# Performance work log

Hardware: AMD Instinct MI355X
Metric: run time of the kernel (lower is better)

The kernel has to match this reference:

```python
import jax, jax.numpy as jnp
import numpy as np

N = 50000      # nodes
E = 800000     # edges
IN = 64        # in_channels
HID = 256      # hidden_dim
LAT = 64       # latent_dim
KS = 2         # kernel_size per dim
DIM = 3        # pseudo-coordinate dim
K = KS ** DIM  # 8 spline weight matrices


def spline_basis_coeffs(pseudo, ks, dim, dtype):
    """Degree-1 open B-spline basis: returns per-edge coefficients c [E, ks**dim]."""
    e = pseudo.shape[0]
    v = pseudo * (ks - 1)                                   # [E, dim]
    bot = jnp.clip(jnp.floor(v), 0, ks - 1).astype(jnp.int32)
    frac = v - bot
    c = jnp.zeros((e, ks ** dim), dtype)
    rows = jnp.arange(e)
    for s in range(2 ** dim):  # 8 knot combinations (fixed small loop)
        w = jnp.ones(e, dtype)
        idx = jnp.zeros(e, jnp.int32)
        for d in range(dim):
            bit = (s >> d) & 1
            w = w * (frac[:, d] if bit else 1.0 - frac[:, d])
            idx = idx + jnp.clip(bot[:, d] + bit, 0, ks - 1) * (ks ** d)
        c = c.at[rows, idx].add(w)
    return c


def spline_conv(x, edge_index, pseudo, W, Wroot, b):
    """SplineConv with aggr='mean', root weight and bias (degree-1 open splines)."""
    src, dst = edge_index[0], edge_index[1]
    n = x.shape[0]
    e = pseudo.shape[0]
    c = spline_basis_coeffs(pseudo, KS, DIM, x.dtype)        # [E, K]
    x_src = x[src]                                           # [E, in] gather
    deg = jax.ops.segment_sum(jnp.ones(e, x.dtype), dst, num_segments=n)
    inv_deg = (1.0 / jnp.maximum(deg, 1.0))[:, None]         # [N, 1] mean aggr
    out = jnp.zeros((n, W.shape[2]), x.dtype)
    for k in range(W.shape[0]):  # K=8 fixed loop; scatter-add then dense matmul
        agg = jax.ops.segment_sum(c[:, k:k + 1] * x_src, dst, num_segments=n)
        out = out + (agg * inv_deg) @ W[k]
    return out + x @ Wroot + b


def setup_inputs() -> dict:
    key = jax.random.key(0)
    ks = jax.random.split(key, 12)
    x = jax.random.normal(ks[0], (N, IN), jnp.float32)
    edge_index = jax.random.randint(ks[1], (2, E), 0, N, jnp.int32)
    s = 0.05
    return {
        "x": x,
        "edge_index": edge_index,
        "conv1_W": jax.random.normal(ks[2], (K, IN, HID), jnp.float32) * s,
        "conv1_root": jax.random.normal(ks[3], (IN, HID), jnp.float32) * s,
        "conv1_b": jnp.zeros((HID,), jnp.float32),
        "conv2_W": jax.random.normal(ks[4], (K, HID, LAT), jnp.float32) * s,
        "conv2_root": jax.random.normal(ks[5], (HID, LAT), jnp.float32) * s,
        "conv2_b": jnp.zeros((LAT,), jnp.float32),
        "dec_w1": jax.random.normal(ks[6], (LAT, HID), jnp.float32) * s,
        "dec_b1": jnp.zeros((HID,), jnp.float32),
        "dec_w2": jax.random.normal(ks[7], (HID, IN), jnp.float32) * s,
        "dec_b2": jnp.zeros((IN,), jnp.float32),
    }


def reference(x, edge_index, conv1_W, conv1_root, conv1_b,
              conv2_W, conv2_root, conv2_b,
              dec_w1, dec_b1, dec_w2, dec_b2):
    pseudo = jnp.zeros((edge_index.shape[1], DIM), x.dtype)  # forward builds zeros
    h = jax.nn.relu(spline_conv(x, edge_index, pseudo, conv1_W, conv1_root, conv1_b))
    z = spline_conv(h, edge_index, pseudo, conv2_W, conv2_root, conv2_b)
    h2 = jax.nn.relu(z @ dec_w1 + dec_b1)
    return h2 @ dec_w2 + dec_b2
```

## Files before the change

### kernel.cpp

```cpp
#include <hip/hip_runtime.h>
#include <hip/hip_bf16.h>


#define THREADS 256

typedef __attribute__((ext_vector_type(8))) short bf16x8;
typedef __attribute__((ext_vector_type(4))) float f32x4;

__device__ __forceinline__ float bf2f(unsigned short u) {
    unsigned v = ((unsigned)u) << 16;
    return __builtin_bit_cast(float, v);
}
__device__ __forceinline__ unsigned short f2bf(float f) {
    __hip_bfloat16 h = __float2bfloat16(f);
    return __builtin_bit_cast(unsigned short, h);
}
__device__ __forceinline__ void acc4(float* f, uint2 v) {
    f[0] += bf2f((unsigned short)v.x);
    f[1] += bf2f((unsigned short)(v.x >> 16));
    f[2] += bf2f((unsigned short)v.y);
    f[3] += bf2f((unsigned short)(v.y >> 16));
}

__device__ __forceinline__ void pack_one(unsigned short* dst,
                                         const float* W0, const float* W1,
                                         int NB, int ksplit, int colsplit,
                                         int ld0, int ld1, int t) {
    int i = t & 7, lane = (t >> 3) & 63, rest = t >> 9;
    int j = rest % NB, s = rest / NB;
    int k = s * 32 + ((lane >> 4) << 3) + i;
    int c = (j << 4) + (lane & 15);
    float v;
    if (c >= colsplit)    v = W1[(size_t)k * ld1 + (c - colsplit)];
    else if (k >= ksplit) v = W1[(size_t)(k - ksplit) * ld1 + c];
    else                  v = W0[(size_t)k * ld0 + c];
    dst[t] = f2bf(v);
}

#define BIG (1 << 30)

__global__ void prep_kernel(const float* __restrict__ W1g, const float* __restrict__ root1,
                            const float* __restrict__ W2g, const float* __restrict__ root2,
                            const float* __restrict__ dw1, const float* __restrict__ dw2,
                            const float* __restrict__ x, const int* __restrict__ dstv,
                            int* __restrict__ bcnt,
                            unsigned short* __restrict__ Pb1,
                            unsigned short* __restrict__ Pb2,
                            unsigned short* __restrict__ Pd1,
                            unsigned short* __restrict__ Pd2,
                            unsigned short* __restrict__ ab1,
                            int n, int E, int pb_pack) {
    if ((int)blockIdx.x >= pb_pack) {
        __shared__ int hist[256];
        int t = threadIdx.x;
        hist[t] = 0;
        __syncthreads();
        int e0 = ((int)blockIdx.x - pb_pack) * 4096;
#pragma unroll
        for (int i = 0; i < 16; ++i) {
            int e = e0 + t + i * 256;
            if (e < E) atomicAdd(&hist[dstv[e] >> 8], 1);
        }
        __syncthreads();
        int h = hist[t];
        if (h) atomicAdd(&bcnt[t], h);
        return;
    }
    int t = blockIdx.x * blockDim.x + threadIdx.x;
    if (t < 32768) {
        pack_one(Pb1, W1g, root1, 16, 64, BIG, 256, 256, t);
    } else if (t < 65536) {
        pack_one(Pb2, W2g, root2, 8, BIG, 64, 64, 64, t - 32768);
    } else if (t < 81920) {
        pack_one(Pd1, dw1, dw1, 16, BIG, BIG, 256, 256, t - 65536);
    } else if (t < 98304) {
        pack_one(Pd2, dw2, dw2, 4, BIG, BIG, 64, 64, t - 81920);
    } else if (t < 98304 + n * 16) {
        int u = t - 98304;
        int row = u >> 4, c4 = (u & 15) * 4;
        float4 v = *(const float4*)(x + (size_t)row * 64 + c4);
        unsigned lo = (unsigned)f2bf(v.x) | ((unsigned)f2bf(v.y) << 16);
        unsigned hi = (unsigned)f2bf(v.z) | ((unsigned)f2bf(v.w) << 16);
        uint2 o; o.x = lo; o.y = hi;
        *(uint2*)(ab1 + (size_t)row * 128 + 64 + c4) = o;
    }
}

__global__ __launch_bounds__(256) void partition_edges(
    const int* __restrict__ src, const int* __restrict__ dst,
    const int* __restrict__ bcnt, int* __restrict__ bcur,
    int* __restrict__ epack, int E) {
    __shared__ int hist[256];
    __shared__ int base[256];
    __shared__ int lcur[256];
    __shared__ int bb[256];
    int t = threadIdx.x;
    hist[t] = 0;
    __syncthreads();
    int e0 = blockIdx.x * 4096;
    int myd[16], mys[16];
#pragma unroll
    for (int i = 0; i < 16; ++i) {
        int e = e0 + t + i * 256;
        int d = (e < E) ? dst[e] : -1;
        mys[i] = (e < E) ? src[e] : 0;
        myd[i] = d;
        if (d >= 0) atomicAdd(&hist[d >> 8], 1);
    }
    int cb = bcnt[t];
    bb[t] = cb;
    __syncthreads();
    for (int off = 1; off < 256; off <<= 1) {
        int xv = (t >= off) ? bb[t - off] : 0;
        __syncthreads();
        bb[t] += xv;
        __syncthreads();
    }
    int bbase_t = bb[t] - cb;
    int h = hist[t];
    if (h > 0) base[t] = bbase_t + atomicAdd(&bcur[t], h);
    lcur[t] = 0;
    __syncthreads();
#pragma unroll
    for (int i = 0; i < 16; ++i) {
        int d = myd[i];
        if (d >= 0) {
            int b = d >> 8;
            int p = atomicAdd(&lcur[b], 1);
            epack[base[b] + p] = ((d & 255) << 20) | mys[i];
        }
    }
}

__global__ __launch_bounds__(256) void bucket_fill2(
    const int* __restrict__ epack, const int* __restrict__ bcnt,
    int* __restrict__ offs, float* __restrict__ invd,
    int* __restrict__ esrc, int N) {
    __shared__ int sb_[256];
    __shared__ int nh[256];
    __shared__ int loff[256];
    __shared__ int ncur[256];
    __shared__ int stage[8192];
    int b = blockIdx.x, t = threadIdx.x;
    int n0 = b << 8;
    int cntn = min(256, N - n0);
    int cb = bcnt[t];
    sb_[t] = cb;
    __syncthreads();
    for (int off = 1; off < 256; off <<= 1) {
        int xv = (t >= off) ? sb_[t - off] : 0;
        __syncthreads();
        sb_[t] += xv;
        __syncthreads();
    }
    int ebase = b ? sb_[b - 1] : 0;
    int ecount = sb_[b] - ebase;
    if (b == 0 && t == 0) offs[N] = sb_[255];
    nh[t] = 0;
    __syncthreads();
    for (int i = t; i < ecount; i += 256)
        atomicAdd(&nh[epack[ebase + i] >> 20], 1);
    __syncthreads();
    int v = nh[t];
    loff[t] = v;
    __syncthreads();
    for (int off = 1; off < 256; off <<= 1) {
        int xv = (t >= off) ? loff[t - off] : 0;
        __syncthreads();
        loff[t] += xv;
        __syncthreads();
    }
    int ex = loff[t] - v;
    loff[t] = ex;
    if (t < cntn) {
        offs[n0 + t] = ebase + ex;
        invd[n0 + t] = 1.0f / (float)max(v, 1);
    }
    ncur[t] = 0;
    __syncthreads();
    bool useLds = (ecount <= 8192);
    for (int i = t; i < ecount; i += 256) {
        int p = epack[ebase + i];
        int dl = p >> 20;
        int pos = atomicAdd(&ncur[dl], 1);
        int g = loff[dl] + pos;
        int sv = p & 0xFFFFF;
        if (useLds) stage[g] = sv;
        else        esrc[ebase + g] = sv;
    }
    __syncthreads();
    if (useLds)
        for (int i = t; i < ecount; i += 256) esrc[ebase + i] = stage[i];
}

__global__ void agg_x4(unsigned short* __restrict__ ab1, const int* __restrict__ esrc,
                       const int* __restrict__ offs, const float* __restrict__ invd,
                       int n) {
    int node = blockIdx.x * 4 + (threadIdx.x >> 6);
    if (node >= n) return;
    int l = threadIdx.x & 63;
    int slot = l >> 4, c = l & 15;
    const unsigned short* xb = ab1 + 64 + c * 4;
    int s = offs[node], e = offs[node + 1];
    float a0[4] = {}, a1[4] = {}, a2[4] = {}, a3[4] = {};
    int j = s;
    for (; j + 16 <= e; j += 16) {
        int i0 = esrc[j + slot],      i1 = esrc[j + 4 + slot];
        int i2 = esrc[j + 8 + slot],  i3 = esrc[j + 12 + slot];
        uint2 v0 = *(const uint2*)(xb + (size_t)i0 * 128);
        uint2 v1 = *(const uint2*)(xb + (size_t)i1 * 128);
        uint2 v2 = *(const uint2*)(xb + (size_t)i2 * 128);
        uint2 v3 = *(const uint2*)(xb + (size_t)i3 * 128);
        acc4(a0, v0); acc4(a1, v1); acc4(a2, v2); acc4(a3, v3);
    }
    for (; j + 4 <= e; j += 4) {
        int i0 = esrc[j + slot];
        uint2 v0 = *(const uint2*)(xb + (size_t)i0 * 128);
        acc4(a0, v0);
    }
    int rem = e - j;
    if (slot < rem) {
        int i0 = esrc[j + slot];
        uint2 v0 = *(const uint2*)(xb + (size_t)i0 * 128);
        acc4(a1, v0);
    }
    float r[4];
#pragma unroll
    for (int k = 0; k < 4; ++k) {
        r[k] = (a0[k] + a1[k]) + (a2[k] + a3[k]);
        r[k] += __shfl_xor(r[k], 16);
        r[k] += __shfl_xor(r[k], 32);
    }
    if (slot == 0) {
        float iv = invd[node];
        unsigned lo = (unsigned)f2bf(r[0] * iv) | ((unsigned)f2bf(r[1] * iv) << 16);
        unsigned hi = (unsigned)f2bf(r[2] * iv) | ((unsigned)f2bf(r[3] * iv) << 16);
        uint2 o; o.x = lo; o.y = hi;
        *(uint2*)(ab1 + (size_t)node * 128 + c * 4) = o;
    }
}

__global__ void agg_z4(const unsigned short* __restrict__ hwroot,
                       const int* __restrict__ esrc, const int* __restrict__ offs,
                       const float* __restrict__ invd, const float* __restrict__ b2,
                       unsigned short* __restrict__ z, int n) {
    int node = blockIdx.x * 4 + (threadIdx.x >> 6);
    if (node >= n) return;
    int l = threadIdx.x & 63;
    int slot = l >> 4, c = l & 15;
    const unsigned short* hb = hwroot + c * 4;
    int s = offs[node], e = offs[node + 1];
    float a0[4] = {}, a1[4] = {}, a2[4] = {}, a3[4] = {};
    int j = s;
    for (; j + 16 <= e; j += 16) {
        int i0 = esrc[j + slot],      i1 = esrc[j + 4 + slot];
        int i2 = esrc[j + 8 + slot],  i3 = esrc[j + 12 + slot];
        uint2 v0 = *(const uint2*)(hb + (size_t)i0 * 128);
        uint2 v1 = *(const uint2*)(hb + (size_t)i1 * 128);
        uint2 v2 = *(const uint2*)(hb + (size_t)i2 * 128);
        uint2 v3 = *(const uint2*)(hb + (size_t)i3 * 128);
        acc4(a0, v0); acc4(a1, v1); acc4(a2, v2); acc4(a3, v3);
    }
    for (; j + 4 <= e; j += 4) {
        int i0 = esrc[j + slot];
        uint2 v0 = *(const uint2*)(hb + (size_t)i0 * 128);
        acc4(a0, v0);
    }
    int rem = e - j;
    if (slot < rem) {
        int i0 = esrc[j + slot];
        uint2 v0 = *(const uint2*)(hb + (size_t)i0 * 128);
        acc4(a1, v0);
    }
    float r[4];
#pragma unroll
    for (int k = 0; k < 4; ++k) {
        r[k] = (a0[k] + a1[k]) + (a2[k] + a3[k]);
        r[k] += __shfl_xor(r[k], 16);
        r[k] += __shfl_xor(r[k], 32);
    }
    if (slot == 0) {
        float iv = invd[node];
        uint2 hr = *(const uint2*)(hwroot + (size_t)node * 128 + 64 + c * 4);
        float v0 = r[0] * iv + bf2f((unsigned short)hr.x) + b2[c * 4 + 0];
        float v1 = r[1] * iv + bf2f((unsigned short)(hr.x >> 16)) + b2[c * 4 + 1];
        float v2 = r[2] * iv + bf2f((unsigned short)hr.y) + b2[c * 4 + 2];
        float v3 = r[3] * iv + bf2f((unsigned short)(hr.y >> 16)) + b2[c * 4 + 3];
        unsigned lo = (unsigned)f2bf(v0) | ((unsigned)f2bf(v1) << 16);
        unsigned hi = (unsigned)f2bf(v2) | ((unsigned)f2bf(v3) << 16);
        uint2 o; o.x = lo; o.y = hi;
        *(uint2*)(z + (size_t)node * 64 + c * 4) = o;
    }
}

template <int K1, int NBW2, bool OUTBF>
__global__ __launch_bounds__(256) void gemm_fused(
    const unsigned short* __restrict__ A,
    const unsigned short* __restrict__ Bp1, const float* __restrict__ bias1,
    const unsigned short* __restrict__ Bp2, const float* __restrict__ bias2,
    void* __restrict__ Cv, int n)
{
    constexpr int KS1 = K1 / 32;
    constexpr int N2 = NBW2 * 64;
    constexpr int NB2 = NBW2 * 4;
    __shared__ unsigned short ht[64][264];

    const int m0 = blockIdx.x * 64;
    const int lane = threadIdx.x & 63;
    const int w = threadIdx.x >> 6;
    const int quad = lane >> 4;
    const int l16 = lane & 15;

    {
        f32x4 acc[4][4] = {};
        const unsigned short* Arow = A + (size_t)(m0 + l16) * K1 + quad * 8;
        for (int s = 0; s < KS1; ++s) {
            bf16x8 a[4];
#pragma unroll
            for (int mb = 0; mb < 4; ++mb)
                a[mb] = *(const bf16x8*)(Arow + (size_t)mb * 16 * K1 + s * 32);
#pragma unroll
            for (int jn = 0; jn < 4; ++jn) {
                int j = w * 4 + jn;
                bf16x8 b = *(const bf16x8*)(Bp1 + ((size_t)(s * 16 + j) * 64 + lane) * 8);
#pragma unroll
                for (int mb = 0; mb < 4; ++mb)
                    acc[mb][jn] = __builtin_amdgcn_mfma_f32_16x16x32_bf16(a[mb], b, acc[mb][jn], 0, 0, 0);
            }
        }
#pragma unroll
        for (int jn = 0; jn < 4; ++jn) {
            int col = (w * 4 + jn) * 16 + l16;
            float bv = bias1[col];
#pragma unroll
            for (int mb = 0; mb < 4; ++mb)
#pragma unroll
                for (int r = 0; r < 4; ++r) {
                    int row = mb * 16 + quad * 4 + r;
                    ht[row][col] = f2bf(fmaxf(acc[mb][jn][r] + bv, 0.f));
                }
        }
    }
    __syncthreads();

    {
        f32x4 acc[4][NBW2] = {};
        for (int s = 0; s < 8; ++s) {
            bf16x8 a[4];
#pragma unroll
            for (int mb = 0; mb < 4; ++mb)
                a[mb] = *(const bf16x8*)&ht[mb * 16 + l16][s * 32 + quad * 8];
#pragma unroll
            for (int jn = 0; jn < NBW2; ++jn) {
                int j = w * NBW2 + jn;
                bf16x8 b = *(const bf16x8*)(Bp2 + ((size_t)(s * NB2 + j) * 64 + lane) * 8);
#pragma unroll
                for (int mb = 0; mb < 4; ++mb)
                    acc[mb][jn] = __builtin_amdgcn_mfma_f32_16x16x32_bf16(a[mb], b, acc[mb][jn], 0, 0, 0);
            }
        }
#pragma unroll
        for (int jn = 0; jn < NBW2; ++jn) {
            int col = (w * NBW2 + jn) * 16 + l16;
            float bv = bias2 ? bias2[col] : 0.f;
#pragma unroll
            for (int mb = 0; mb < 4; ++mb)
#pragma unroll
                for (int r = 0; r < 4; ++r) {
                    int row = m0 + mb * 16 + quad * 4 + r;
                    if (row < n) {
                        float v = acc[mb][jn][r] + bv;
                        if (OUTBF)
                            ((unsigned short*)Cv)[(size_t)row * N2 + col] = f2bf(v);
                        else
                            ((float*)Cv)[(size_t)row * N2 + col] = v;
                    }
                }
        }
    }
}

extern "C" void kernel_launch(void* const* d_in, const int* in_sizes, int n_in,
                              void* d_out, int out_size, void* d_ws, size_t ws_size,
                              hipStream_t stream) {
    const float* x      = (const float*)d_in[0];
    const int*   ei     = (const int*)d_in[1];
    const float* W1g    = (const float*)d_in[2];
    const float* root1  = (const float*)d_in[3];
    const float* b1     = (const float*)d_in[4];
    const float* W2g    = (const float*)d_in[5];
    const float* root2  = (const float*)d_in[6];
    const float* b2     = (const float*)d_in[7];
    const float* dw1    = (const float*)d_in[8];
    const float* db1    = (const float*)d_in[9];
    const float* dw2    = (const float*)d_in[10];
    const float* db2    = (const float*)d_in[11];
    float* out = (float*)d_out;

    const int N = in_sizes[0] / 64;
    const int E = in_sizes[1] / 2;
    const int Npad = N + 64;
    const int* srcv = ei;
    const int* dstv = ei + E;

    char* ws = (char*)d_ws;
    auto alloc = [&](size_t bytes) -> void* {
        void* p = (void*)ws;
        ws += (bytes + 255) & ~(size_t)255;
        return p;
    };
    int*   bcnt   = (int*)alloc(1024);
    int*   bcur   = (int*)alloc(1024);
    int*   offs   = (int*)alloc((size_t)(N + 1) * 4);
    float* invd   = (float*)alloc((size_t)N * 4);
    int*   esrc   = (int*)alloc((size_t)E * 4);
    int*   epack  = (int*)alloc((size_t)E * 4);
    unsigned short* Pb1 = (unsigned short*)alloc(32768 * 2);
    unsigned short* Pb2 = (unsigned short*)alloc(32768 * 2);
    unsigned short* Pd1 = (unsigned short*)alloc(16384 * 2);
    unsigned short* Pd2 = (unsigned short*)alloc(16384 * 2);
    unsigned short* ab1    = (unsigned short*)alloc((size_t)Npad * 128 * 2);
    unsigned short* hwroot = (unsigned short*)alloc((size_t)Npad * 128 * 2);
    unsigned short* z      = (unsigned short*)alloc((size_t)Npad * 64 * 2);

    hipMemsetAsync(bcnt, 0, 2048, stream);

    int gb = (N + 63) / 64;
    int nbkt = (N + 255) / 256;
    int pa = (E + 4095) / 4096;
    int pb_pack = (98304 + N * 16 + THREADS - 1) / THREADS;

    prep_kernel<<<pb_pack + pa, THREADS, 0, stream>>>(
        W1g, root1, W2g, root2, dw1, dw2, x, dstv, bcnt,
        Pb1, Pb2, Pd1, Pd2, ab1, N, E, pb_pack);
    partition_edges<<<pa, 256, 0, stream>>>(srcv, dstv, bcnt, bcur, epack, E);
    bucket_fill2<<<nbkt, 256, 0, stream>>>(epack, bcnt, offs, invd, esrc, N);

    agg_x4<<<(N + 3) / 4, THREADS, 0, stream>>>(ab1, esrc, offs, invd, N);
    gemm_fused<128, 2, true><<<gb, 256, 0, stream>>>(ab1, Pb1, b1, Pb2, nullptr, hwroot, N);
    agg_z4<<<(N + 3) / 4, THREADS, 0, stream>>>(hwroot, esrc, offs, invd, b2, z, N);
    gemm_fused<64, 1, false><<<gb, 256, 0, stream>>>(z, Pd1, db1, Pd2, db2, out, N);
}
```

Before: 209.3 us.

## Fuse neighbor aggregation into GEMM kernels via LDS staging

The separate aggregation kernels are folded into the two fused GEMM kernels. Each 64-row block first gathers and mean-aggregates its own nodes' neighbor features into shared memory, then runs the MFMA matmuls from LDS. The gather is also widened from 8-byte to 16-byte loads with 8 edge slots per wave. This removes two launches and the global round-trip of the aggregated tensors and z. The trade-off is that the gather phase now runs with GEMM-sized grids (fewer blocks) and waves serialize 16 passes per block, which may reduce latency hiding for the irregular gathers.

```diff
diff --git a/kernel.cpp b/kernel.cpp
--- a/kernel.cpp
+++ b/kernel.cpp
@@ -15,11 +15,11 @@
     __hip_bfloat16 h = __float2bfloat16(f);
     return __builtin_bit_cast(unsigned short, h);
 }
-__device__ __forceinline__ void acc4(float* f, uint2 v) {
-    f[0] += bf2f((unsigned short)v.x);
-    f[1] += bf2f((unsigned short)(v.x >> 16));
-    f[2] += bf2f((unsigned short)v.y);
-    f[3] += bf2f((unsigned short)(v.y >> 16));
+__device__ __forceinline__ void acc8(float* f, uint4 v) {
+    f[0] += bf2f((unsigned short)v.x); f[1] += bf2f((unsigned short)(v.x >> 16));
+    f[2] += bf2f((unsigned short)v.y); f[3] += bf2f((unsigned short)(v.y >> 16));
+    f[4] += bf2f((unsigned short)v.z); f[5] += bf2f((unsigned short)(v.z >> 16));
+    f[6] += bf2f((unsigned short)v.w); f[7] += bf2f((unsigned short)(v.w >> 16));
 }
 
 __device__ __forceinline__ void pack_one(unsigned short* dst,
@@ -193,118 +193,47 @@
         for (int i = t; i < ecount; i += 256) esrc[ebase + i] = stage[i];
 }
 
-__global__ void agg_x4(unsigned short* __restrict__ ab1, const int* __restrict__ esrc,
-                       const int* __restrict__ offs, const float* __restrict__ invd,
-                       int n) {
-    int node = blockIdx.x * 4 + (threadIdx.x >> 6);
-    if (node >= n) return;
-    int l = threadIdx.x & 63;
-    int slot = l >> 4, c = l & 15;
-    const unsigned short* xb = ab1 + 64 + c * 4;
-    int s = offs[node], e = offs[node + 1];
-    float a0[4] = {}, a1[4] = {}, a2[4] = {}, a3[4] = {};
-    int j = s;
-    for (; j + 16 <= e; j += 16) {
-        int i0 = esrc[j + slot],      i1 = esrc[j + 4 + slot];
-        int i2 = esrc[j + 8 + slot],  i3 = esrc[j + 12 + slot];
-        uint2 v0 = *(const uint2*)(xb + (size_t)i0 * 128);
-        uint2 v1 = *(const uint2*)(xb + (size_t)i1 * 128);
-        uint2 v2 = *(const uint2*)(xb + (size_t)i2 * 128);
-        uint2 v3 = *(const uint2*)(xb + (size_t)i3 * 128);
-        acc4(a0, v0); acc4(a1, v1); acc4(a2, v2); acc4(a3, v3);
-    }
-    for (; j + 4 <= e; j += 4) {
+__device__ __forceinline__ void gather_node(const unsigned short* __restrict__ tb,
+                                            const int* __restrict__ esrc,
+                                            int s0, int e0, int slot, float* r) {
+    float a0[8] = {}, a1[8] = {};
+    int j = s0;
+    for (; j + 16 <= e0; j += 16) {
+        int i0 = esrc[j + slot], i1 = esrc[j + 8 + slot];
+        uint4 v0 = *(const uint4*)(tb + (size_t)i0 * 128);
+        uint4 v1 = *(const uint4*)(tb + (size_t)i1 * 128);
+        acc8(a0, v0); acc8(a1, v1);
+    }
+    if (j + 8 <= e0) {
         int i0 = esrc[j + slot];
-        uint2 v0 = *(const uint2*)(xb + (size_t)i0 * 128);
-        acc4(a0, v0);
-    }
-    int rem = e - j;
-    if (slot < rem) {
+        uint4 v0 = *(const uint4*)(tb + (size_t)i0 * 128);
+        acc8(a0, v0);
+        j += 8;
+    }
+    if (slot < e0 - j) {
         int i0 = esrc[j + slot];
-        uint2 v0 = *(const uint2*)(xb + (size_t)i0 * 128);
-        acc4(a1, v0);
-    }
-    float r[4];
-#pragma unroll
-    for (int k = 0; k < 4; ++k) {
-        r[k] = (a0[k] + a1[k]) + (a2[k] + a3[k]);
+        uint4 v0 = *(const uint4*)(tb + (size_t)i0 * 128);
+        acc8(a1, v0);
+    }
+#pragma unroll
+    for (int k = 0; k < 8; ++k) {
+        r[k] = a0[k] + a1[k];
+        r[k] += __shfl_xor(r[k], 8);
         r[k] += __shfl_xor(r[k], 16);
         r[k] += __shfl_xor(r[k], 32);
     }
-    if (slot == 0) {
-        float iv = invd[node];
-        unsigned lo = (unsigned)f2bf(r[0] * iv) | ((unsigned)f2bf(r[1] * iv) << 16);
-        unsigned hi = (unsigned)f2bf(r[2] * iv) | ((unsigned)f2bf(r[3] * iv) << 16);
-        uint2 o; o.x = lo; o.y = hi;
-        *(uint2*)(ab1 + (size_t)node * 128 + c * 4) = o;
-    }
-}
-
-__global__ void agg_z4(const unsigned short* __restrict__ hwroot,
-                       const int* __restrict__ esrc, const int* __restrict__ offs,
-                       const float* __restrict__ invd, const float* __restrict__ b2,
-                       unsigned short* __restrict__ z, int n) {
-    int node = blockIdx.x * 4 + (threadIdx.x >> 6);
-    if (node >= n) return;
-    int l = threadIdx.x & 63;
-    int slot = l >> 4, c = l & 15;
-    const unsigned short* hb = hwroot + c * 4;
-    int s = offs[node], e = offs[node + 1];
-    float a0[4] = {}, a1[4] = {}, a2[4] = {}, a3[4] = {};
-    int j = s;
-    for (; j + 16 <= e; j += 16) {
-        int i0 = esrc[j + slot],      i1 = esrc[j + 4 + slot];
-        int i2 = esrc[j + 8 + slot],  i3 = esrc[j + 12 + slot];
-        uint2 v0 = *(const uint2*)(hb + (size_t)i0 * 128);
-        uint2 v1 = *(const uint2*)(hb + (size_t)i1 * 128);
-        uint2 v2 = *(const uint2*)(hb + (size_t)i2 * 128);
-        uint2 v3 = *(const uint2*)(hb + (size_t)i3 * 128);
-        acc4(a0, v0); acc4(a1, v1); acc4(a2, v2); acc4(a3, v3);
-    }
-    for (; j + 4 <= e; j += 4) {
-        int i0 = esrc[j + slot];
-        uint2 v0 = *(const uint2*)(hb + (size_t)i0 * 128);
-        acc4(a0, v0);
-    }
-    int rem = e - j;
-    if (slot < rem) {
-        int i0 = esrc[j + slot];
-        uint2 v0 = *(const uint2*)(hb + (size_t)i0 * 128);
-        acc4(a1, v0);
-    }
-    float r[4];
-#pragma unroll
-    for (int k = 0; k < 4; ++k) {
-        r[k] = (a0[k] + a1[k]) + (a2[k] + a3[k]);
-        r[k] += __shfl_xor(r[k], 16);
-        r[k] += __shfl_xor(r[k], 32);
-    }
-    if (slot == 0) {
-        float iv = invd[node];
-        uint2 hr = *(const uint2*)(hwroot + (size_t)node * 128 + 64 + c * 4);
-        float v0 = r[0] * iv + bf2f((unsigned short)hr.x) + b2[c * 4 + 0];
-        float v1 = r[1] * iv + bf2f((unsigned short)(hr.x >> 16)) + b2[c * 4 + 1];
-        float v2 = r[2] * iv + bf2f((unsigned short)hr.y) + b2[c * 4 + 2];
-        float v3 = r[3] * iv + bf2f((unsigned short)(hr.y >> 16)) + b2[c * 4 + 3];
-        unsigned lo = (unsigned)f2bf(v0) | ((unsigned)f2bf(v1) << 16);
-        unsigned hi = (unsigned)f2bf(v2) | ((unsigned)f2bf(v3) << 16);
-        uint2 o; o.x = lo; o.y = hi;
-        *(uint2*)(z + (size_t)node * 64 + c * 4) = o;
-    }
-}
-
-template <int K1, int NBW2, bool OUTBF>
-__global__ __launch_bounds__(256) void gemm_fused(
-    const unsigned short* __restrict__ A,
+}
+
+__global__ __launch_bounds__(256) void gemm1_fused(
+    const unsigned short* __restrict__ ab1,
+    const int* __restrict__ esrc, const int* __restrict__ offs,
+    const float* __restrict__ invd,
     const unsigned short* __restrict__ Bp1, const float* __restrict__ bias1,
-    const unsigned short* __restrict__ Bp2, const float* __restrict__ bias2,
-    void* __restrict__ Cv, int n)
+    const unsigned short* __restrict__ Bp2,
+    unsigned short* __restrict__ hwroot, int n)
 {
-    constexpr int KS1 = K1 / 32;
-    constexpr int N2 = NBW2 * 64;
-    constexpr int NB2 = NBW2 * 4;
+    __shared__ unsigned short at[64][72];
     __shared__ unsigned short ht[64][264];
-
     const int m0 = blockIdx.x * 64;
     const int lane = threadIdx.x & 63;
     const int w = threadIdx.x >> 6;
@@ -312,13 +241,40 @@
     const int l16 = lane & 15;
 
     {
+        const int slot = lane >> 3, c = lane & 7;
+        const unsigned short* tb = ab1 + 64 + c * 8;
+        for (int pass = 0; pass < 16; ++pass) {
+            int node = m0 + (pass << 2) + w;
+            if (node >= n) continue;
+            int s0 = offs[node], e0 = offs[node + 1];
+            float r[8];
+            gather_node(tb, esrc, s0, e0, slot, r);
+            if (slot == 0) {
+                float iv = invd[node];
+                unsigned p0 = (unsigned)f2bf(r[0] * iv) | ((unsigned)f2bf(r[1] * iv) << 16);
+                unsigned p1 = (unsigned)f2bf(r[2] * iv) | ((unsigned)f2bf(r[3] * iv) << 16);
+                unsigned p2 = (unsigned)f2bf(r[4] * iv) | ((unsigned)f2bf(r[5] * iv) << 16);
+                unsigned p3 = (unsigned)f2bf(r[6] * iv) | ((unsigned)f2bf(r[7] * iv) << 16);
+                uint4 o; o.x = p0; o.y = p1; o.z = p2; o.w = p3;
+                *(uint4*)&at[(pass << 2) + w][c * 8] = o;
+            }
+        }
+    }
+    __syncthreads();
+
+    {
         f32x4 acc[4][4] = {};
-        const unsigned short* Arow = A + (size_t)(m0 + l16) * K1 + quad * 8;
-        for (int s = 0; s < KS1; ++s) {
+        const unsigned short* xrow = ab1 + (size_t)(m0 + l16) * 128 + 64 + quad * 8;
+#pragma unroll
+        for (int s = 0; s < 4; ++s) {
             bf16x8 a[4];
 #pragma unroll
-            for (int mb = 0; mb < 4; ++mb)
-                a[mb] = *(const bf16x8*)(Arow + (size_t)mb * 16 * K1 + s * 32);
+            for (int mb = 0; mb < 4; ++mb) {
+                if (s < 2)
+                    a[mb] = *(const bf16x8*)&at[mb * 16 + l16][s * 32 + quad * 8];
+                else
+                    a[mb] = *(const bf16x8*)(xrow + (size_t)mb * 16 * 128 + (s - 2) * 32);
+            }
 #pragma unroll
             for (int jn = 0; jn < 4; ++jn) {
                 int j = w * 4 + jn;
@@ -344,39 +300,139 @@
     __syncthreads();
 
     {
-        f32x4 acc[4][NBW2] = {};
+        f32x4 acc[4][2] = {};
         for (int s = 0; s < 8; ++s) {
             bf16x8 a[4];
 #pragma unroll
             for (int mb = 0; mb < 4; ++mb)
                 a[mb] = *(const bf16x8*)&ht[mb * 16 + l16][s * 32 + quad * 8];
 #pragma unroll
-            for (int jn = 0; jn < NBW2; ++jn) {
-                int j = w * NBW2 + jn;
-                bf16x8 b = *(const bf16x8*)(Bp2 + ((size_t)(s * NB2 + j) * 64 + lane) * 8);
+            for (int jn = 0; jn < 2; ++jn) {
+                int j = w * 2 + jn;
+                bf16x8 b = *(const bf16x8*)(Bp2 + ((size_t)(s * 8 + j) * 64 + lane) * 8);
 #pragma unroll
                 for (int mb = 0; mb < 4; ++mb)
                     acc[mb][jn] = __builtin_amdgcn_mfma_f32_16x16x32_bf16(a[mb], b, acc[mb][jn], 0, 0, 0);
             }
         }
 #pragma unroll
-        for (int jn = 0; jn < NBW2; ++jn) {
-            int col = (w * NBW2 + jn) * 16 + l16;
-            float bv = bias2 ? bias2[col] : 0.f;
+        for (int jn = 0; jn < 2; ++jn) {
+            int col = (w * 2 + jn) * 16 + l16;
 #pragma unroll
             for (int mb = 0; mb < 4; ++mb)
 #pragma unroll
                 for (int r = 0; r < 4; ++r) {
                     int row = m0 + mb * 16 + quad * 4 + r;
-                    if (row < n) {
-                        float v = acc[mb][jn][r] + bv;
-                        if (OUTBF)
-                            ((unsigned short*)Cv)[(size_t)row * N2 + col] = f2bf(v);
-                        else
-                            ((float*)Cv)[(size_t)row * N2 + col] = v;
-                    }
+                    if (row < n)
+                        hwroot[(size_t)row * 128 + col] = f2bf(acc[mb][jn][r]);
                 }
         }
+    }
+}
+
+__global__ __launch_bounds__(256) void gemm2_fused(
+    const unsigned short* __restrict__ hwroot,
+    const int* __restrict__ esrc, const int* __restrict__ offs,
+    const float* __restrict__ invd, const float* __restrict__ b2,
+    const unsigned short* __restrict__ Pd1, const float* __restrict__ db1,
+    const unsigned short* __restrict__ Pd2, const float* __restrict__ db2,
+    float* __restrict__ out, int n)
+{
+    __shared__ unsigned short zt[64][72];
+    __shared__ unsigned short ht[64][264];
+    const int m0 = blockIdx.x * 64;
+    const int lane = threadIdx.x & 63;
+    const int w = threadIdx.x >> 6;
+    const int quad = lane >> 4;
+    const int l16 = lane & 15;
+
+    {
+        const int slot = lane >> 3, c = lane & 7;
+        const unsigned short* tb = hwroot + c * 8;
+        for (int pass = 0; pass < 16; ++pass) {
+            int node = m0 + (pass << 2) + w;
+            if (node >= n) continue;
+            int s0 = offs[node], e0 = offs[node + 1];
+            float r[8];
+            gather_node(tb, esrc, s0, e0, slot, r);
+            if (slot == 0) {
+                float iv = invd[node];
+                uint4 hr = *(const uint4*)(hwroot + (size_t)node * 128 + 64 + c * 8);
+                float4 bA = *(const float4*)(b2 + c * 8);
+                float4 bB = *(const float4*)(b2 + c * 8 + 4);
+                float v0 = r[0] * iv + bf2f((unsigned short)hr.x) + bA.x;
+                float v1 = r[1] * iv + bf2f((unsigned short)(hr.x >> 16)) + bA.y;
+                float v2 = r[2] * iv + bf2f((unsigned short)hr.y) + bA.z;
+                float v3 = r[3] * iv + bf2f((unsigned short)(hr.y >> 16)) + bA.w;
+                float v4 = r[4] * iv + bf2f((unsigned short)hr.z) + bB.x;
+                float v5 = r[5] * iv + bf2f((unsigned short)(hr.z >> 16)) + bB.y;
+                float v6 = r[6] * iv + bf2f((unsigned short)hr.w) + bB.z;
+                float v7 = r[7] * iv + bf2f((unsigned short)(hr.w >> 16)) + bB.w;
+                unsigned p0 = (unsigned)f2bf(v0) | ((unsigned)f2bf(v1) << 16);
+                unsigned p1 = (unsigned)f2bf(v2) | ((unsigned)f2bf(v3) << 16);
+                unsigned p2 = (unsigned)f2bf(v4) | ((unsigned)f2bf(v5) << 16);
+                unsigned p3 = (unsigned)f2bf(v6) | ((unsigned)f2bf(v7) << 16);
+                uint4 o; o.x = p0; o.y = p1; o.z = p2; o.w = p3;
+                *(uint4*)&zt[(pass << 2) + w][c * 8] = o;
+            }
+        }
+    }
+    __syncthreads();
+
+    {
+        f32x4 acc[4][4] = {};
+#pragma unroll
+        for (int s = 0; s < 2; ++s) {
+            bf16x8 a[4];
+#pragma unroll
+            for (int mb = 0; mb < 4; ++mb)
+                a[mb] = *(const bf16x8*)&zt[mb * 16 + l16][s * 32 + quad * 8];
+#pragma unroll
+            for (int jn = 0; jn < 4; ++jn) {
+                int j = w * 4 + jn;
+                bf16x8 b = *(const bf16x8*)(Pd1 + ((size_t)(s * 16 + j) * 64 + lane) * 8);
+#pragma unroll
+                for (int mb = 0; mb < 4; ++mb)
+                    acc[mb][jn] = __builtin_amdgcn_mfma_f32_16x16x32_bf16(a[mb], b, acc[mb][jn], 0, 0, 0);
+            }
+        }
+#pragma unroll
+        for (int jn = 0; jn < 4; ++jn) {
+            int col = (w * 4 + jn) * 16 + l16;
+            float bv = db1[col];
+#pragma unroll
+            for (int mb = 0; mb < 4; ++mb)
+#pragma unroll
+                for (int r = 0; r < 4; ++r) {
+                    int row = mb * 16 + quad * 4 + r;
+                    ht[row][col] = f2bf(fmaxf(acc[mb][jn][r] + bv, 0.f));
+                }
+        }
+    }
+    __syncthreads();
+
+    {
+        f32x4 acc[4] = {};
+        for (int s = 0; s < 8; ++s) {
+            bf16x8 a[4];
+#pragma unroll
+            for (int mb = 0; mb < 4; ++mb)
+                a[mb] = *(const bf16x8*)&ht[mb * 16 + l16][s * 32 + quad * 8];
+            bf16x8 b = *(const bf16x8*)(Pd2 + ((size_t)(s * 4 + w) * 64 + lane) * 8);
+#pragma unroll
+            for (int mb = 0; mb < 4; ++mb)
+                acc[mb] = __builtin_amdgcn_mfma_f32_16x16x32_bf16(a[mb], b, acc[mb], 0, 0, 0);
+        }
+        int col = w * 16 + l16;
+        float bv = db2[col];
+#pragma unroll
+        for (int mb = 0; mb < 4; ++mb)
+#pragma unroll
+            for (int r = 0; r < 4; ++r) {
+                int row = m0 + mb * 16 + quad * 4 + r;
+                if (row < n)
+                    out[(size_t)row * 64 + col] = acc[mb][r] + bv;
+            }
     }
 }
 
@@ -421,7 +477,6 @@
     unsigned short* Pd2 = (unsigned short*)alloc(16384 * 2);
     unsigned short* ab1    = (unsigned short*)alloc((size_t)Npad * 128 * 2);
     unsigned short* hwroot = (unsigned short*)alloc((size_t)Npad * 128 * 2);
-    unsigned short* z      = (unsigned short*)alloc((size_t)Npad * 64 * 2);
 
     hipMemsetAsync(bcnt, 0, 2048, stream);
 
@@ -436,8 +491,7 @@
     partition_edges<<<pa, 256, 0, stream>>>(srcv, dstv, bcnt, bcur, epack, E);
     bucket_fill2<<<nbkt, 256, 0, stream>>>(epack, bcnt, offs, invd, esrc, N);
 
-    agg_x4<<<(N + 3) / 4, THREADS, 0, stream>>>(ab1, esrc, offs, invd, N);
-    gemm_fused<128, 2, true><<<gb, 256, 0, stream>>>(ab1, Pb1, b1, Pb2, nullptr, hwroot, N);
-    agg_z4<<<(N + 3) / 4, THREADS, 0, stream>>>(hwroot, esrc, offs, invd, b2, z, N);
-    gemm_fused<64, 1, false><<<gb, 256, 0, stream>>>(z, Pd1, db1, Pd2, db2, out, N);
-}
+    gemm1_fused<<<gb, 256, 0, stream>>>(ab1, esrc, offs, invd, Pb1, b1, Pb2, hwroot, N);
+    gemm2_fused<<<gb, 256, 0, stream>>>(hwroot, esrc, offs, invd, b2,
+                                        Pd1, db1, Pd2, db2, out, N);
+}
```

Result: slower. 278.6 us (+33.1%).

## Replace two-pass bucket CSR build with per-node degree atomics and direct scatter

Applied to the files above, without the earlier changes.

The CSR build now counts per-node degree with global atomics inside the prep kernel. A small kernel scans those counts into offsets, and a scatter kernel places each edge's source index through per-node atomic cursors. This removes the epack intermediate and the bucketed partition/fill passes, at the cost of many contended global atomics and a non-deterministic edge order within each node. Separately, both aggregation kernels switch from 4-wide to 8-wide bf16 gathers (uint4 loads, 8 slots per node instead of 4) to cut load instruction count.

```diff
diff --git a/kernel.cpp b/kernel.cpp
--- a/kernel.cpp
+++ b/kernel.cpp
@@ -15,11 +15,11 @@
     __hip_bfloat16 h = __float2bfloat16(f);
     return __builtin_bit_cast(unsigned short, h);
 }
-__device__ __forceinline__ void acc4(float* f, uint2 v) {
-    f[0] += bf2f((unsigned short)v.x);
-    f[1] += bf2f((unsigned short)(v.x >> 16));
-    f[2] += bf2f((unsigned short)v.y);
-    f[3] += bf2f((unsigned short)(v.y >> 16));
+__device__ __forceinline__ void acc8(float* f, uint4 v) {
+    f[0] += bf2f((unsigned short)v.x); f[1] += bf2f((unsigned short)(v.x >> 16));
+    f[2] += bf2f((unsigned short)v.y); f[3] += bf2f((unsigned short)(v.y >> 16));
+    f[4] += bf2f((unsigned short)v.z); f[5] += bf2f((unsigned short)(v.z >> 16));
+    f[6] += bf2f((unsigned short)v.w); f[7] += bf2f((unsigned short)(v.w >> 16));
 }
 
 __device__ __forceinline__ void pack_one(unsigned short* dst,
@@ -43,7 +43,7 @@
                             const float* __restrict__ W2g, const float* __restrict__ root2,
                             const float* __restrict__ dw1, const float* __restrict__ dw2,
                             const float* __restrict__ x, const int* __restrict__ dstv,
-                            int* __restrict__ bcnt,
+                            int* __restrict__ bcnt, int* __restrict__ deg,
                             unsigned short* __restrict__ Pb1,
                             unsigned short* __restrict__ Pb2,
                             unsigned short* __restrict__ Pd1,
@@ -59,7 +59,11 @@
 #pragma unroll
         for (int i = 0; i < 16; ++i) {
             int e = e0 + t + i * 256;
-            if (e < E) atomicAdd(&hist[dstv[e] >> 8], 1);
+            if (e < E) {
+                int d = dstv[e];
+                atomicAdd(&hist[d >> 8], 1);
+                atomicAdd(&deg[d], 1);
+            }
         }
         __syncthreads();
         int h = hist[t];
@@ -86,66 +90,15 @@
     }
 }
 
-__global__ __launch_bounds__(256) void partition_edges(
-    const int* __restrict__ src, const int* __restrict__ dst,
-    const int* __restrict__ bcnt, int* __restrict__ bcur,
-    int* __restrict__ epack, int E) {
-    __shared__ int hist[256];
-    __shared__ int base[256];
-    __shared__ int lcur[256];
-    __shared__ int bb[256];
-    int t = threadIdx.x;
-    hist[t] = 0;
-    __syncthreads();
-    int e0 = blockIdx.x * 4096;
-    int myd[16], mys[16];
-#pragma unroll
-    for (int i = 0; i < 16; ++i) {
-        int e = e0 + t + i * 256;
-        int d = (e < E) ? dst[e] : -1;
-        mys[i] = (e < E) ? src[e] : 0;
-        myd[i] = d;
-        if (d >= 0) atomicAdd(&hist[d >> 8], 1);
-    }
-    int cb = bcnt[t];
-    bb[t] = cb;
-    __syncthreads();
-    for (int off = 1; off < 256; off <<= 1) {
-        int xv = (t >= off) ? bb[t - off] : 0;
-        __syncthreads();
-        bb[t] += xv;
-        __syncthreads();
-    }
-    int bbase_t = bb[t] - cb;
-    int h = hist[t];
-    if (h > 0) base[t] = bbase_t + atomicAdd(&bcur[t], h);
-    lcur[t] = 0;
-    __syncthreads();
-#pragma unroll
-    for (int i = 0; i < 16; ++i) {
-        int d = myd[i];
-        if (d >= 0) {
-            int b = d >> 8;
-            int p = atomicAdd(&lcur[b], 1);
-            epack[base[b] + p] = ((d & 255) << 20) | mys[i];
-        }
-    }
-}
-
-__global__ __launch_bounds__(256) void bucket_fill2(
-    const int* __restrict__ epack, const int* __restrict__ bcnt,
-    int* __restrict__ offs, float* __restrict__ invd,
-    int* __restrict__ esrc, int N) {
+__global__ __launch_bounds__(256) void build_offs(
+    const int* __restrict__ bcnt, const int* __restrict__ deg,
+    int* __restrict__ offs, int* __restrict__ cur, float* __restrict__ invd,
+    int N, int E) {
     __shared__ int sb_[256];
-    __shared__ int nh[256];
-    __shared__ int loff[256];
-    __shared__ int ncur[256];
-    __shared__ int stage[8192];
+    __shared__ int ld[256];
     int b = blockIdx.x, t = threadIdx.x;
     int n0 = b << 8;
-    int cntn = min(256, N - n0);
-    int cb = bcnt[t];
-    sb_[t] = cb;
+    sb_[t] = bcnt[t];
     __syncthreads();
     for (int off = 1; off < 256; off <<= 1) {
         int xv = (t >= off) ? sb_[t - off] : 0;
@@ -154,43 +107,38 @@
         __syncthreads();
     }
     int ebase = b ? sb_[b - 1] : 0;
-    int ecount = sb_[b] - ebase;
-    if (b == 0 && t == 0) offs[N] = sb_[255];
-    nh[t] = 0;
-    __syncthreads();
-    for (int i = t; i < ecount; i += 256)
-        atomicAdd(&nh[epack[ebase + i] >> 20], 1);
-    __syncthreads();
-    int v = nh[t];
-    loff[t] = v;
+    int node = n0 + t;
+    int d = (node < N) ? deg[node] : 0;
+    ld[t] = d;
     __syncthreads();
     for (int off = 1; off < 256; off <<= 1) {
-        int xv = (t >= off) ? loff[t - off] : 0;
-        __syncthreads();
-        loff[t] += xv;
-        __syncthreads();
-    }
-    int ex = loff[t] - v;
-    loff[t] = ex;
-    if (t < cntn) {
-        offs[n0 + t] = ebase + ex;
-        invd[n0 + t] = 1.0f / (float)max(v, 1);
-    }
-    ncur[t] = 0;
-    __syncthreads();
-    bool useLds = (ecount <= 8192);
-    for (int i = t; i < ecount; i += 256) {
-        int p = epack[ebase + i];
-        int dl = p >> 20;
-        int pos = atomicAdd(&ncur[dl], 1);
-        int g = loff[dl] + pos;
-        int sv = p & 0xFFFFF;
-        if (useLds) stage[g] = sv;
-        else        esrc[ebase + g] = sv;
-    }
-    __syncthreads();
-    if (useLds)
-        for (int i = t; i < ecount; i += 256) esrc[ebase + i] = stage[i];
+        int xv = (t >= off) ? ld[t - off] : 0;
+        __syncthreads();
+        ld[t] += xv;
+        __syncthreads();
+    }
+    int ex = ld[t] - d;
+    if (node < N) {
+        offs[node] = ebase + ex;
+        cur[node]  = ebase + ex;
+        invd[node] = 1.0f / (float)max(d, 1);
+    }
+    if (b == 0 && t == 0) offs[N] = E;
+}
+
+__global__ __launch_bounds__(256) void scatter_edges(
+    const int* __restrict__ src, const int* __restrict__ dst,
+    int* __restrict__ cur, int* __restrict__ esrc, int E) {
+    int e0 = blockIdx.x * 1024 + threadIdx.x;
+#pragma unroll
+    for (int i = 0; i < 4; ++i) {
+        int e = e0 + i * 256;
+        if (e < E) {
+            int d = dst[e];
+            int p = atomicAdd(&cur[d], 1);
+            esrc[p] = src[e];
+        }
+    }
 }
 
 __global__ void agg_x4(unsigned short* __restrict__ ab1, const int* __restrict__ esrc,
@@ -199,44 +147,44 @@
     int node = blockIdx.x * 4 + (threadIdx.x >> 6);
     if (node >= n) return;
     int l = threadIdx.x & 63;
-    int slot = l >> 4, c = l & 15;
-    const unsigned short* xb = ab1 + 64 + c * 4;
+    int slot = l >> 3, c = l & 7;
+    const unsigned short* xb = ab1 + 64 + c * 8;
     int s = offs[node], e = offs[node + 1];
-    float a0[4] = {}, a1[4] = {}, a2[4] = {}, a3[4] = {};
+    float a0[8] = {}, a1[8] = {};
     int j = s;
     for (; j + 16 <= e; j += 16) {
-        int i0 = esrc[j + slot],      i1 = esrc[j + 4 + slot];
-        int i2 = esrc[j + 8 + slot],  i3 = esrc[j + 12 + slot];
-        uint2 v0 = *(const uint2*)(xb + (size_t)i0 * 128);
-        uint2 v1 = *(const uint2*)(xb + (size_t)i1 * 128);
-        uint2 v2 = *(const uint2*)(xb + (size_t)i2 * 128);
-        uint2 v3 = *(const uint2*)(xb + (size_t)i3 * 128);
-        acc4(a0, v0); acc4(a1, v1); acc4(a2, v2); acc4(a3, v3);
-    }
-    for (; j + 4 <= e; j += 4) {
+        int i0 = esrc[j + slot], i1 = esrc[j + 8 + slot];
+        uint4 v0 = *(const uint4*)(xb + (size_t)i0 * 128);
+        uint4 v1 = *(const uint4*)(xb + (size_t)i1 * 128);
+        acc8(a0, v0); acc8(a1, v1);
+    }
+    if (j + 8 <= e) {
         int i0 = esrc[j + slot];
-        uint2 v0 = *(const uint2*)(xb + (size_t)i0 * 128);
-        acc4(a0, v0);
-    }
-    int rem = e - j;
-    if (slot < rem) {
+        uint4 v0 = *(const uint4*)(xb + (size_t)i0 * 128);
+        acc8(a0, v0);
+        j += 8;
+    }
+    if (slot < e - j) {
         int i0 = esrc[j + slot];
-        uint2 v0 = *(const uint2*)(xb + (size_t)i0 * 128);
-        acc4(a1, v0);
-    }
-    float r[4];
-#pragma unroll
-    for (int k = 0; k < 4; ++k) {
-        r[k] = (a0[k] + a1[k]) + (a2[k] + a3[k]);
+        uint4 v0 = *(const uint4*)(xb + (size_t)i0 * 128);
+        acc8(a1, v0);
+    }
+    float r[8];
+#pragma unroll
+    for (int k = 0; k < 8; ++k) {
+        r[k] = a0[k] + a1[k];
+        r[k] += __shfl_xor(r[k], 8);
         r[k] += __shfl_xor(r[k], 16);
         r[k] += __shfl_xor(r[k], 32);
     }
     if (slot == 0) {
         float iv = invd[node];
-        unsigned lo = (unsigned)f2bf(r[0] * iv) | ((unsigned)f2bf(r[1] * iv) << 16);
-        unsigned hi = (unsigned)f2bf(r[2] * iv) | ((unsigned)f2bf(r[3] * iv) << 16);
-        uint2 o; o.x = lo; o.y = hi;
-        *(uint2*)(ab1 + (size_t)node * 128 + c * 4) = o;
+        unsigned p0 = (unsigned)f2bf(r[0] * iv) | ((unsigned)f2bf(r[1] * iv) << 16);
+        unsigned p1 = (unsigned)f2bf(r[2] * iv) | ((unsigned)f2bf(r[3] * iv) << 16);
+        unsigned p2 = (unsigned)f2bf(r[4] * iv) | ((unsigned)f2bf(r[5] * iv) << 16);
+        unsigned p3 = (unsigned)f2bf(r[6] * iv) | ((unsigned)f2bf(r[7] * iv) << 16);
+        uint4 o; o.x = p0; o.y = p1; o.z = p2; o.w = p3;
+        *(uint4*)(ab1 + (size_t)node * 128 + c * 8) = o;
     }
 }
 
@@ -247,49 +195,55 @@
     int node = blockIdx.x * 4 + (threadIdx.x >> 6);
     if (node >= n) return;
     int l = threadIdx.x & 63;
-    int slot = l >> 4, c = l & 15;
-    const unsigned short* hb = hwroot + c * 4;
+    int slot = l >> 3, c = l & 7;
+    const unsigned short* hb = hwroot + c * 8;
     int s = offs[node], e = offs[node + 1];
-    float a0[4] = {}, a1[4] = {}, a2[4] = {}, a3[4] = {};
+    float a0[8] = {}, a1[8] = {};
     int j = s;
     for (; j + 16 <= e; j += 16) {
-        int i0 = esrc[j + slot],      i1 = esrc[j + 4 + slot];
-        int i2 = esrc[j + 8 + slot],  i3 = esrc[j + 12 + slot];
-        uint2 v0 = *(const uint2*)(hb + (size_t)i0 * 128);
-        uint2 v1 = *(const uint2*)(hb + (size_t)i1 * 128);
-        uint2 v2 = *(const uint2*)(hb + (size_t)i2 * 128);
-        uint2 v3 = *(const uint2*)(hb + (size_t)i3 * 128);
-        acc4(a0, v0); acc4(a1, v1); acc4(a2, v2); acc4(a3, v3);
-    }
-    for (; j + 4 <= e; j += 4) {
+        int i0 = esrc[j + slot], i1 = esrc[j + 8 + slot];
+        uint4 v0 = *(const uint4*)(hb + (size_t)i0 * 128);
+        uint4 v1 = *(const uint4*)(hb + (size_t)i1 * 128);
+        acc8(a0, v0); acc8(a1, v1);
+    }
+    if (j + 8 <= e) {
         int i0 = esrc[j + slot];
-        uint2 v0 = *(const uint2*)(hb + (size_t)i0 * 128);
-        acc4(a0, v0);
-    }
-    int rem = e - j;
-    if (slot < rem) {
+        uint4 v0 = *(const uint4*)(hb + (size_t)i0 * 128);
+        acc8(a0, v0);
+        j += 8;
+    }
+    if (slot < e - j) {
         int i0 = esrc[j + slot];
-        uint2 v0 = *(const uint2*)(hb + (size_t)i0 * 128);
-        acc4(a1, v0);
-    }
-    float r[4];
-#pragma unroll
-    for (int k = 0; k < 4; ++k) {
-        r[k] = (a0[k] + a1[k]) + (a2[k] + a3[k]);
+        uint4 v0 = *(const uint4*)(hb + (size_t)i0 * 128);
+        acc8(a1, v0);
+    }
+    float r[8];
+#pragma unroll
+    for (int k = 0; k < 8; ++k) {
+        r[k] = a0[k] + a1[k];
+        r[k] += __shfl_xor(r[k], 8);
         r[k] += __shfl_xor(r[k], 16);
         r[k] += __shfl_xor(r[k], 32);
     }
     if (slot == 0) {
         float iv = invd[node];
-        uint2 hr = *(const uint2*)(hwroot + (size_t)node * 128 + 64 + c * 4);
-        float v0 = r[0] * iv + bf2f((unsigned short)hr.x) + b2[c * 4 + 0];
-        float v1 = r[1] * iv + bf2f((unsigned short)(hr.x >> 16)) + b2[c * 4 + 1];
-        float v2 = r[2] * iv + bf2f((unsigned short)hr.y) + b2[c * 4 + 2];
-        float v3 = r[3] * iv + bf2f((unsigned short)(hr.y >> 16)) + b2[c * 4 + 3];
-        unsigned lo = (unsigned)f2bf(v0) | ((unsigned)f2bf(v1) << 16);
-        unsigned hi = (unsigned)f2bf(v2) | ((unsigned)f2bf(v3) << 16);
-        uint2 o; o.x = lo; o.y = hi;
-        *(uint2*)(z + (size_t)node * 64 + c * 4) = o;
+        uint4 hr = *(const uint4*)(hwroot + (size_t)node * 128 + 64 + c * 8);
+        float4 bA = *(const float4*)(b2 + c * 8);
+        float4 bB = *(const float4*)(b2 + c * 8 + 4);
+        float v0 = r[0] * iv + bf2f((unsigned short)hr.x) + bA.x;
+        float v1 = r[1] * iv + bf2f((unsigned short)(hr.x >> 16)) + bA.y;
+        float v2 = r[2] * iv + bf2f((unsigned short)hr.y) + bA.z;
+        float v3 = r[3] * iv + bf2f((unsigned short)(hr.y >> 16)) + bA.w;
+        float v4 = r[4] * iv + bf2f((unsigned short)hr.z) + bB.x;
+        float v5 = r[5] * iv + bf2f((unsigned short)(hr.z >> 16)) + bB.y;
+        float v6 = r[6] * iv + bf2f((unsigned short)hr.w) + bB.z;
+        float v7 = r[7] * iv + bf2f((unsigned short)(hr.w >> 16)) + bB.w;
+        unsigned p0 = (unsigned)f2bf(v0) | ((unsigned)f2bf(v1) << 16);
+        unsigned p1 = (unsigned)f2bf(v2) | ((unsigned)f2bf(v3) << 16);
+        unsigned p2 = (unsigned)f2bf(v4) | ((unsigned)f2bf(v5) << 16);
+        unsigned p3 = (unsigned)f2bf(v6) | ((unsigned)f2bf(v7) << 16);
+        uint4 o; o.x = p0; o.y = p1; o.z = p2; o.w = p3;
+        *(uint4*)(z + (size_t)node * 64 + c * 8) = o;
     }
 }
 
@@ -410,11 +364,11 @@
         return p;
     };
     int*   bcnt   = (int*)alloc(1024);
-    int*   bcur   = (int*)alloc(1024);
+    int*   deg    = (int*)alloc((size_t)N * 4);
     int*   offs   = (int*)alloc((size_t)(N + 1) * 4);
+    int*   cur    = (int*)alloc((size_t)N * 4);
     float* invd   = (float*)alloc((size_t)N * 4);
     int*   esrc   = (int*)alloc((size_t)E * 4);
-    int*   epack  = (int*)alloc((size_t)E * 4);
     unsigned short* Pb1 = (unsigned short*)alloc(32768 * 2);
     unsigned short* Pb2 = (unsigned short*)alloc(32768 * 2);
     unsigned short* Pd1 = (unsigned short*)alloc(16384 * 2);
@@ -423,7 +377,7 @@
     unsigned short* hwroot = (unsigned short*)alloc((size_t)Npad * 128 * 2);
     unsigned short* z      = (unsigned short*)alloc((size_t)Npad * 64 * 2);
 
-    hipMemsetAsync(bcnt, 0, 2048, stream);
+    hipMemsetAsync(bcnt, 0, 1024 + (size_t)N * 4, stream);
 
     int gb = (N + 63) / 64;
     int nbkt = (N + 255) / 256;
@@ -431,10 +385,10 @@
     int pb_pack = (98304 + N * 16 + THREADS - 1) / THREADS;
 
     prep_kernel<<<pb_pack + pa, THREADS, 0, stream>>>(
-        W1g, root1, W2g, root2, dw1, dw2, x, dstv, bcnt,
+        W1g, root1, W2g, root2, dw1, dw2, x, dstv, bcnt, deg,
         Pb1, Pb2, Pd1, Pd2, ab1, N, E, pb_pack);
-    partition_edges<<<pa, 256, 0, stream>>>(srcv, dstv, bcnt, bcur, epack, E);
-    bucket_fill2<<<nbkt, 256, 0, stream>>>(epack, bcnt, offs, invd, esrc, N);
+    build_offs<<<nbkt, 256, 0, stream>>>(bcnt, deg, offs, cur, invd, N, E);
+    scatter_edges<<<(E + 1023) / 1024, 256, 0, stream>>>(srcv, dstv, cur, esrc, E);
 
     agg_x4<<<(N + 3) / 4, THREADS, 0, stream>>>(ab1, esrc, offs, invd, N);
     gemm_fused<128, 2, true><<<gb, 256, 0, stream>>>(ab1, Pb1, b1, Pb2, nullptr, hwroot, N);
```

Result: slower. 264.4 us (+26.3%).
